# Performance work log

Measured on AMD Instinct MI355X. Metric: run time of the kernel, lower is better.

## Reference

```python
import jax, jax.numpy as jnp
import numpy as np

N_NODES, SEQ, FEAT, HID, NLAYERS = 126, 24, 17, 100, 2


def setup_inputs() -> dict:
    key = jax.random.key(0)
    ks = jax.random.split(key, 14)
    B = 64
    s = 1.0 / np.sqrt(HID)  # torch LSTM default init scale
    inp = {
        "x": jax.random.normal(ks[0], (B, SEQ, N_NODES, FEAT), dtype=jnp.float32),
        # per-node stacked LSTM weights, gate order (i, f, g, o) as in torch
        "W_ih0": jax.random.uniform(ks[1], (N_NODES, 4 * HID, FEAT), jnp.float32, -s, s),
        "W_hh0": jax.random.uniform(ks[2], (N_NODES, 4 * HID, HID), jnp.float32, -s, s),
        "b_ih0": jax.random.uniform(ks[3], (N_NODES, 4 * HID), jnp.float32, -s, s),
        "b_hh0": jax.random.uniform(ks[4], (N_NODES, 4 * HID), jnp.float32, -s, s),
        "W_ih1": jax.random.uniform(ks[5], (N_NODES, 4 * HID, HID), jnp.float32, -s, s),
        "W_hh1": jax.random.uniform(ks[6], (N_NODES, 4 * HID, HID), jnp.float32, -s, s),
        "b_ih1": jax.random.uniform(ks[7], (N_NODES, 4 * HID), jnp.float32, -s, s),
        "b_hh1": jax.random.uniform(ks[8], (N_NODES, 4 * HID), jnp.float32, -s, s),
        "w_lin": jax.random.uniform(ks[9], (1, HID), jnp.float32, -s, s),
        "b_lin": jax.random.uniform(ks[10], (1,), jnp.float32, -s, s),
        "w_end": jax.random.uniform(ks[11], (1, SEQ), jnp.float32, -0.2, 0.2),  # Conv2d(seqlen->1, k=1)
        "b_end": jax.random.uniform(ks[12], (1,), jnp.float32, -0.2, 0.2),
    }
    return inp


def _lstm_cell(xin, h, c, Wih, Whh, bih, bhh):
    # xin: [N,B,Fin], h/c: [N,B,H], Wih: [N,4H,Fin], Whh: [N,4H,H]
    g = (jnp.einsum("nbf,ngf->nbg", xin, Wih)
         + jnp.einsum("nbh,ngh->nbg", h, Whh)
         + (bih + bhh)[:, None, :])
    i, f, gg, o = jnp.split(g, 4, axis=-1)
    c_new = jax.nn.sigmoid(f) * c + jax.nn.sigmoid(i) * jnp.tanh(gg)
    h_new = jax.nn.sigmoid(o) * jnp.tanh(c_new)
    return h_new, c_new


def reference(x, W_ih0, W_hh0, b_ih0, b_hh0, W_ih1, W_hh1, b_ih1, b_hh1,
              w_lin, b_lin, w_end, b_end):
    B, T, N, F = x.shape
    H = W_hh0.shape[-1]
    xt = jnp.transpose(x, (1, 2, 0, 3))  # [T, N, B, F]
    z = jnp.zeros((N, B, H), dtype=x.dtype)

    def step(carry, x_t):
        h1, c1, h2, c2 = carry
        h1, c1 = _lstm_cell(x_t, h1, c1, W_ih0, W_hh0, b_ih0, b_hh0)
        h2, c2 = _lstm_cell(h1, h2, c2, W_ih1, W_hh1, b_ih1, b_hh1)
        return (h1, c1, h2, c2), h2

    (h1, c1, h2, c2), outs = jax.lax.scan(step, (z, z, z, z), xt)  # outs: [T,N,B,H]
    lin = jnp.einsum("tnbh,oh->tnbo", outs, w_lin) + b_lin  # [T,N,B,1]
    lstmlayer = jnp.transpose(lin, (2, 0, 1, 3))  # [B,T,N,1] (matches torch permute(2,1,0,3))
    # Conv2d(seqlen -> out_channels=1, kernel 1x1) over the T channel axis
    out = jnp.einsum("btnj,ct->bcnj", lstmlayer, w_end) + b_end[None, :, None, None]  # [B,1,N,1]
    hn = jnp.stack([h1, h2], axis=1)  # [N, num_layers=2, B, H]
    cn = jnp.stack([c1, c2], axis=1)
    return (out, hn, cn)
```

## Files before the change

kernel.cpp:

```cpp
#include <hip/hip_runtime.h>
#include <hip/hip_bf16.h>

#define NN 126
#define TT 24
#define FF 17
#define HH 100
#define NMT 25

#define AL_SH 51200
#define X0_SH AL_SH
#define X1_SH (AL_SH + 8192)
#define X0BUF 4096
#define X1BUF 7168
#define TOT_SH (X1_SH + 2 * X1BUF)
#define LDS_BYTES (TOT_SH * 2)

typedef __attribute__((ext_vector_type(8))) short short8v;
typedef __attribute__((ext_vector_type(4))) float float4v;

__device__ __forceinline__ short f2bf(float f) {
    union { float f; unsigned u; } v; v.f = f;
    unsigned r = v.u + 0x7FFFu + ((v.u >> 16) & 1u);
    return (short)(r >> 16);
}
#define LOG2E 1.4426950408889634f
__device__ __forceinline__ float sigm_(float x) {
    return __builtin_amdgcn_rcpf(1.0f + __builtin_amdgcn_exp2f(-LOG2E * x));
}
__device__ __forceinline__ float tanh_(float x) {
    return 1.0f - 2.0f * __builtin_amdgcn_rcpf(1.0f + __builtin_amdgcn_exp2f((2.0f * LOG2E) * x));
}

__global__ __launch_bounds__(1024, 4)
void lstm_skew(const float* __restrict__ x,
               const float* __restrict__ Wih0, const float* __restrict__ Whh0,
               const float* __restrict__ bih0, const float* __restrict__ bhh0,
               const float* __restrict__ Wih1, const float* __restrict__ Whh1,
               const float* __restrict__ bih1, const float* __restrict__ bhh1,
               const float* __restrict__ wlin, const float* __restrict__ blin,
               const float* __restrict__ wend, const float* __restrict__ bend,
               float* __restrict__ out)
{
    extern __shared__ short lds_s[];
    short* Al = lds_s;
    short* X0 = lds_s + X0_SH;
    short* X1 = lds_s + X1_SH;
    float* red = (float*)lds_s;

    const int n   = blockIdx.x >> 1;
    const int bh  = blockIdx.x & 1;
    const int tid = threadIdx.x, lane = tid & 63, w = tid >> 6;
    const int cl  = lane & 15, q = lane >> 4;
    const int mt0 = (w <= 8) ? (w * 2) : (18 + (w - 9));
    const int nmt = (w <= 8) ? 2 : 1;

    {
        const short8v zz = {0,0,0,0,0,0,0,0};
        for (int i = tid; i < TOT_SH / 8; i += 1024)
            *(short8v*)(lds_s + (size_t)i * 8) = zz;
    }
    __syncthreads();

    {
        const float* W = Whh0 + (size_t)n * 40000;
        for (int i = tid; i < 40000; i += 1024) {
            const int orl = i / 100, j = i - orl * 100;
            const int g = orl / 100, cell = orl - g * 100;
            const int gr = cell * 4 + g;
            const int k = 18 + j;
            Al[(((k >> 5) * NMT + (gr >> 4)) * 64 + ((((k >> 3) & 3) << 4) | (gr & 15))) * 8 + (k & 7)]
                = f2bf(W[i]);
        }
    }
    {
        const float* W = Wih0 + (size_t)n * 6800;
        for (int i = tid; i < 6800; i += 1024) {
            const int orl = i / 17, k = i - orl * 17;
            const int g = orl / 100, cell = orl - g * 100;
            const int gr = cell * 4 + g;
            Al[((gr >> 4) * 64 + ((((k >> 3) & 3) << 4) | (gr & 15))) * 8 + (k & 7)] = f2bf(W[i]);
        }
    }
    if (tid < 400) {
        const int g = tid / 100, cell = tid - g * 100;
        const int gr = cell * 4 + g;
        const int orow = n * 400 + tid;
        Al[((gr >> 4) * 64 + ((2 << 4) | (gr & 15))) * 8 + 1] = f2bf(bih0[orow] + bhh0[orow]);
    }

    short8v wreg[2][7];
    #pragma unroll
    for (int mi = 0; mi < 2; ++mi) {
        if (mi < nmt) {
            const int gr = (mt0 + mi) * 16 + cl;
            const int cell = gr >> 2, g = gr & 3;
            const int orow = n * 400 + g * HH + cell;
            const float* Wi = Wih1 + (size_t)orow * HH;
            const float* Wh = Whh1 + (size_t)orow * HH;
            #pragma unroll
            for (int kt = 0; kt < 7; ++kt) {
                const int k0 = kt * 32 + q * 8;
                float v[8];
                #pragma unroll
                for (int e = 0; e < 8; ++e) v[e] = 0.0f;
                if (k0 == 0) {
                    v[0] = bih1[orow] + bhh1[orow];
                    v[4] = Wi[0]; v[5] = Wi[1]; v[6] = Wi[2]; v[7] = Wi[3];
                } else if (k0 <= 96) {
                    #pragma unroll
                    for (int e = 0; e < 8; ++e) v[e] = Wi[k0 - 4 + e];
                } else if (k0 >= 104 && k0 <= 192) {
                    #pragma unroll
                    for (int e = 0; e < 8; ++e) v[e] = Wh[k0 - 104 + e];
                } else if (k0 == 200) {
                    v[0] = Wh[96]; v[1] = Wh[97]; v[2] = Wh[98]; v[3] = Wh[99];
                }
                short8v pv;
                #pragma unroll
                for (int e = 0; e < 8; ++e) pv[e] = f2bf(v[e]);
                wreg[mi][kt] = pv;
            }
        }
    }

    int aX0h1[2][2], aX1h1[2][2], aX1h2[2][2];
    #pragma unroll
    for (int mi = 0; mi < 2; ++mi) {
        const int cell = (mt0 + mi) * 4 + q;
        #pragma unroll
        for (int nh = 0; nh < 2; ++nh) {
            { const int k = 18 + cell;
              aX0h1[mi][nh] = (((k >> 5) * 2 + nh) * 64 + ((((k >> 3) & 3) << 4) | cl)) * 8 + (k & 7); }
            { const int k = 4 + cell;
              aX1h1[mi][nh] = (((k >> 5) * 2 + nh) * 64 + ((((k >> 3) & 3) << 4) | cl)) * 8 + (k & 7); }
            { const int k = 104 + cell;
              aX1h2[mi][nh] = (((k >> 5) * 2 + nh) * 64 + ((((k >> 3) & 3) << 4) | cl)) * 8 + (k & 7); }
        }
    }
    __syncthreads();

    if (tid < 32) {
        const int off = (((tid >> 4)) * 64 + (tid & 15)) * 8 + 0;
        X1[off] = (short)0x3F80;
        X1[X1BUF + off] = (short)0x3F80;
    }
    if (w < 2) {
        const int b = bh * 32 + w * 16 + cl;
        const float* xr = x + ((size_t)b * TT + 0) * (NN * FF) + n * FF;
        if (q < 2) {
            short8v pv;
            #pragma unroll
            for (int e = 0; e < 8; ++e) pv[e] = f2bf(xr[q * 8 + e]);
            *(short8v*)(X0 + ((size_t)w * 64 + lane) * 8) = pv;
        } else if (q == 2) {
            const unsigned lo = (unsigned short)f2bf(xr[16]);
            *(unsigned*)(X0 + ((size_t)w * 64 + lane) * 8) = (0x3F80u << 16) | lo;
        }
    }
    __syncthreads();

    float c1[2][2], c2[2][2], macc[2][2];
    #pragma unroll
    for (int mi = 0; mi < 2; ++mi)
        #pragma unroll
        for (int nh = 0; nh < 2; ++nh) { c1[mi][nh] = 0.f; c2[mi][nh] = 0.f; macc[mi][nh] = 0.f; }

    for (int i = 0; i <= TT; ++i) {
        const int rb = i & 1;
        const int wb = rb ^ 1;
        float4v acc[2][2];

        if (i < TT) {
            float xv0 = 0.f, xv1 = 0.f, xv2 = 0.f, xv3 = 0.f, xv4 = 0.f, xv5 = 0.f, xv6 = 0.f, xv7 = 0.f;
            const bool doX = (w < 2) && (i + 1 < TT);
            if (doX) {
                const int b = bh * 32 + w * 16 + cl;
                const float* xr = x + ((size_t)b * TT + (i + 1)) * (NN * FF) + n * FF;
                if (q < 2) {
                    const int k0 = q * 8;
                    xv0 = xr[k0 + 0]; xv1 = xr[k0 + 1]; xv2 = xr[k0 + 2]; xv3 = xr[k0 + 3];
                    xv4 = xr[k0 + 4]; xv5 = xr[k0 + 5]; xv6 = xr[k0 + 6]; xv7 = xr[k0 + 7];
                } else if (q == 2) {
                    xv0 = xr[16];
                }
            }

            #pragma unroll
            for (int mi = 0; mi < 2; ++mi) { acc[mi][0] = (float4v){0,0,0,0}; acc[mi][1] = (float4v){0,0,0,0}; }
            {
                const short* X0r = X0 + rb * X0BUF;
                #pragma unroll
                for (int kt = 0; kt < 4; ++kt) {
                    const short8v b0 = *(const short8v*)(X0r + (((size_t)kt * 2 + 0) * 64 + lane) * 8);
                    const short8v b1 = *(const short8v*)(X0r + (((size_t)kt * 2 + 1) * 64 + lane) * 8);
                    #pragma unroll
                    for (int mi = 0; mi < 2; ++mi) {
                        if (mi < nmt) {
                            const short8v a = *(const short8v*)(
                                Al + (((size_t)kt * NMT + (mt0 + mi)) * 64 + lane) * 8);
                            acc[mi][0] = __builtin_amdgcn_mfma_f32_16x16x32_bf16(a, b0, acc[mi][0], 0, 0, 0);
                            acc[mi][1] = __builtin_amdgcn_mfma_f32_16x16x32_bf16(a, b1, acc[mi][1], 0, 0, 0);
                        }
                    }
                }
            }
            const bool fin0 = (i == TT - 1);
            #pragma unroll
            for (int mi = 0; mi < 2; ++mi) {
                if (mi < nmt) {
                    const int cell = (mt0 + mi) * 4 + q;
                    #pragma unroll
                    for (int nh = 0; nh < 2; ++nh) {
                        const float iv = sigm_(acc[mi][nh][0]);
                        const float fv = sigm_(acc[mi][nh][1]);
                        const float gv = tanh_(acc[mi][nh][2]);
                        const float ov = sigm_(acc[mi][nh][3]);
                        const float c  = fv * c1[mi][nh] + iv * gv;
                        c1[mi][nh] = c;
                        const float h = ov * tanh_(c);
                        const short hb = f2bf(h);
                        X0[wb * X0BUF + aX0h1[mi][nh]] = hb;
                        X1[wb * X1BUF + aX1h1[mi][nh]] = hb;
                        if (fin0) {
                            const int b = bh * 32 + nh * 16 + cl;
                            out[8064 + ((size_t)(n * 2 + 0) * 64 + b) * HH + cell] = h;
                            out[8064 + 1612800 + ((size_t)(n * 2 + 0) * 64 + b) * HH + cell] = c;
                        }
                    }
                }
            }
            if (doX) {
                short* X0w = X0 + wb * X0BUF;
                if (q < 2) {
                    short8v pv;
                    pv[0] = f2bf(xv0); pv[1] = f2bf(xv1); pv[2] = f2bf(xv2); pv[3] = f2bf(xv3);
                    pv[4] = f2bf(xv4); pv[5] = f2bf(xv5); pv[6] = f2bf(xv6); pv[7] = f2bf(xv7);
                    *(short8v*)(X0w + ((size_t)w * 64 + lane) * 8) = pv;
                } else if (q == 2) {
                    const unsigned lo = (unsigned short)f2bf(xv0);
                    *(unsigned*)(X0w + ((size_t)w * 64 + lane) * 8) = (0x3F80u << 16) | lo;
                }
            }
        }

        if (i > 0) {
            #pragma unroll
            for (int mi = 0; mi < 2; ++mi) { acc[mi][0] = (float4v){0,0,0,0}; acc[mi][1] = (float4v){0,0,0,0}; }
            {
                const short* X1r = X1 + rb * X1BUF;
                #pragma unroll
                for (int kt = 0; kt < 7; ++kt) {
                    const short8v b0 = *(const short8v*)(X1r + (((size_t)kt * 2 + 0) * 64 + lane) * 8);
                    const short8v b1 = *(const short8v*)(X1r + (((size_t)kt * 2 + 1) * 64 + lane) * 8);
                    #pragma unroll
                    for (int mi = 0; mi < 2; ++mi) {
                        if (mi < nmt) {
                            acc[mi][0] = __builtin_amdgcn_mfma_f32_16x16x32_bf16(wreg[mi][kt], b0, acc[mi][0], 0, 0, 0);
                            acc[mi][1] = __builtin_amdgcn_mfma_f32_16x16x32_bf16(wreg[mi][kt], b1, acc[mi][1], 0, 0, 0);
                        }
                    }
                }
            }
            const float wet = wend[i - 1];
            const bool fin1 = (i == TT);
            #pragma unroll
            for (int mi = 0; mi < 2; ++mi) {
                if (mi < nmt) {
                    const int cell = (mt0 + mi) * 4 + q;
                    #pragma unroll
                    for (int nh = 0; nh < 2; ++nh) {
                        const float iv = sigm_(acc[mi][nh][0]);
                        const float fv = sigm_(acc[mi][nh][1]);
                        const float gv = tanh_(acc[mi][nh][2]);
                        const float ov = sigm_(acc[mi][nh][3]);
                        const float c  = fv * c2[mi][nh] + iv * gv;
                        c2[mi][nh] = c;
                        const float h = ov * tanh_(c);
                        macc[mi][nh] = fmaf(wet, h, macc[mi][nh]);
                        if (!fin1) X1[wb * X1BUF + aX1h2[mi][nh]] = f2bf(h);
                        if (fin1) {
                            const int b = bh * 32 + nh * 16 + cl;
                            out[8064 + ((size_t)(n * 2 + 1) * 64 + b) * HH + cell] = h;
                            out[8064 + 1612800 + ((size_t)(n * 2 + 1) * 64 + b) * HH + cell] = c;
                        }
                    }
                }
            }
        }
        __syncthreads();
    }

    #pragma unroll
    for (int mi = 0; mi < 2; ++mi) {
        if (mi < nmt) {
            const int cell = (mt0 + mi) * 4 + q;
            #pragma unroll
            for (int nh = 0; nh < 2; ++nh)
                red[cell * 32 + nh * 16 + cl] = wlin[cell] * macc[mi][nh];
        }
    }
    __syncthreads();
    if (tid < 32) {
        float s = 0.0f;
        for (int j = 0; j < HH; ++j) s += red[j * 32 + tid];
        float ws = 0.0f;
        for (int t2 = 0; t2 < TT; ++t2) ws += wend[t2];
        s += blin[0] * ws + bend[0];
        out[(size_t)(bh * 32 + tid) * NN + n] = s;
    }
}

extern "C" void kernel_launch(void* const* d_in, const int* in_sizes, int n_in,
                              void* d_out, int out_size, void* d_ws, size_t ws_size,
                              hipStream_t stream) {
    const float* x    = (const float*)d_in[0];
    const float* Wih0 = (const float*)d_in[1];
    const float* Whh0 = (const float*)d_in[2];
    const float* bih0 = (const float*)d_in[3];
    const float* bhh0 = (const float*)d_in[4];
    const float* Wih1 = (const float*)d_in[5];
    const float* Whh1 = (const float*)d_in[6];
    const float* bih1 = (const float*)d_in[7];
    const float* bhh1 = (const float*)d_in[8];
    const float* wlin = (const float*)d_in[9];
    const float* blin = (const float*)d_in[10];
    const float* wend = (const float*)d_in[11];
    const float* bend = (const float*)d_in[12];
    (void)d_ws; (void)ws_size; (void)in_sizes; (void)n_in; (void)out_size;

    lstm_skew<<<dim3(NN * 2), dim3(1024), LDS_BYTES, stream>>>(
        x, Wih0, Whh0, bih0, bhh0, Wih1, Whh1, bih1, bhh1,
        wlin, blin, wend, bend, (float*)d_out);
}
```

Before: 116.1 us.

## Halve block to 512 threads, give each wave more tiles, overlap layer MFMAs

Shrinks the block from 16 to 8 waves, so each wave owns 3 M-tiles (the last wave owns 4). Layer-1 weights for the extra tile are staged in a new LDS region instead of registers. Both layers' MFMA phases are now issued back-to-back before either gate activation, so the two matrix chains can interleave. This trades fewer waves and higher per-wave register pressure for more independent MFMA work per wave and less waiting between phases.

```diff
diff --git a/kernel.cpp b/kernel.cpp
--- a/kernel.cpp
+++ b/kernel.cpp
@@ -7,12 +7,13 @@
 #define HH 100
 #define NMT 25
 
-#define AL_SH 51200
-#define X0_SH AL_SH
-#define X1_SH (AL_SH + 8192)
+#define AL_SH   51200
+#define B24_SH  (AL_SH)
+#define X0_SH   (AL_SH + 3584)
+#define X1_SH   (X0_SH + 8192)
 #define X0BUF 4096
 #define X1BUF 7168
-#define TOT_SH (X1_SH + 2 * X1BUF)
+#define TOT_SH  (X1_SH + 2 * X1BUF)
 #define LDS_BYTES (TOT_SH * 2)
 
 typedef __attribute__((ext_vector_type(8))) short short8v;
@@ -31,39 +32,41 @@
     return 1.0f - 2.0f * __builtin_amdgcn_rcpf(1.0f + __builtin_amdgcn_exp2f((2.0f * LOG2E) * x));
 }
 
-__global__ __launch_bounds__(1024, 4)
-void lstm_skew(const float* __restrict__ x,
-               const float* __restrict__ Wih0, const float* __restrict__ Whh0,
-               const float* __restrict__ bih0, const float* __restrict__ bhh0,
-               const float* __restrict__ Wih1, const float* __restrict__ Whh1,
-               const float* __restrict__ bih1, const float* __restrict__ bhh1,
-               const float* __restrict__ wlin, const float* __restrict__ blin,
-               const float* __restrict__ wend, const float* __restrict__ bend,
-               float* __restrict__ out)
+__global__ __launch_bounds__(512, 2)
+void lstm_ovl(const float* __restrict__ x,
+              const float* __restrict__ Wih0, const float* __restrict__ Whh0,
+              const float* __restrict__ bih0, const float* __restrict__ bhh0,
+              const float* __restrict__ Wih1, const float* __restrict__ Whh1,
+              const float* __restrict__ bih1, const float* __restrict__ bhh1,
+              const float* __restrict__ wlin, const float* __restrict__ blin,
+              const float* __restrict__ wend, const float* __restrict__ bend,
+              float* __restrict__ out)
 {
     extern __shared__ short lds_s[];
-    short* Al = lds_s;
-    short* X0 = lds_s + X0_SH;
-    short* X1 = lds_s + X1_SH;
-    float* red = (float*)lds_s;
+    short* Al   = lds_s;
+    short* B24l = lds_s + B24_SH;
+    short* X0   = lds_s + X0_SH;
+    short* X1   = lds_s + X1_SH;
+    float* red  = (float*)lds_s;
 
     const int n   = blockIdx.x >> 1;
     const int bh  = blockIdx.x & 1;
     const int tid = threadIdx.x, lane = tid & 63, w = tid >> 6;
     const int cl  = lane & 15, q = lane >> 4;
-    const int mt0 = (w <= 8) ? (w * 2) : (18 + (w - 9));
-    const int nmt = (w <= 8) ? 2 : 1;
+    const int mt0 = w * 3;
+    const bool w7 = (w == 7);
+    const int nmt = w7 ? 4 : 3;
 
     {
         const short8v zz = {0,0,0,0,0,0,0,0};
-        for (int i = tid; i < TOT_SH / 8; i += 1024)
+        for (int i = tid; i < TOT_SH / 8; i += 512)
             *(short8v*)(lds_s + (size_t)i * 8) = zz;
     }
     __syncthreads();
 
     {
         const float* W = Whh0 + (size_t)n * 40000;
-        for (int i = tid; i < 40000; i += 1024) {
+        for (int i = tid; i < 40000; i += 512) {
             const int orl = i / 100, j = i - orl * 100;
             const int g = orl / 100, cell = orl - g * 100;
             const int gr = cell * 4 + g;
@@ -74,7 +77,7 @@
     }
     {
         const float* W = Wih0 + (size_t)n * 6800;
-        for (int i = tid; i < 6800; i += 1024) {
+        for (int i = tid; i < 6800; i += 512) {
             const int orl = i / 17, k = i - orl * 17;
             const int g = orl / 100, cell = orl - g * 100;
             const int gr = cell * 4 + g;
@@ -87,45 +90,63 @@
         const int orow = n * 400 + tid;
         Al[((gr >> 4) * 64 + ((2 << 4) | (gr & 15))) * 8 + 1] = f2bf(bih0[orow] + bhh0[orow]);
     }
-
-    short8v wreg[2][7];
+    for (int i = tid; i < 7 * 64; i += 512) {
+        const int kt = i >> 6, l = i & 63;
+        const int row16 = l & 15, kq = l >> 4;
+        const int gr = 24 * 16 + row16;
+        const int cell = gr >> 2, g = gr & 3;
+        const int orow = n * 400 + g * HH + cell;
+        const float* Wi = Wih1 + (size_t)orow * HH;
+        const float* Wh = Whh1 + (size_t)orow * HH;
+        short8v pv;
+        #pragma unroll
+        for (int e = 0; e < 8; ++e) {
+            const int k = kt * 32 + kq * 8 + e;
+            float f = 0.0f;
+            if (k == 0)                      f = bih1[orow] + bhh1[orow];
+            else if (k >= 4 && k < 4 + HH)   f = Wi[k - 4];
+            else if (k >= 104 && k < 104+HH) f = Wh[k - 104];
+            pv[e] = f2bf(f);
+        }
+        *(short8v*)(B24l + (size_t)i * 8) = pv;
+    }
+
+    short8v wr1[3][7];
     #pragma unroll
-    for (int mi = 0; mi < 2; ++mi) {
-        if (mi < nmt) {
-            const int gr = (mt0 + mi) * 16 + cl;
-            const int cell = gr >> 2, g = gr & 3;
-            const int orow = n * 400 + g * HH + cell;
-            const float* Wi = Wih1 + (size_t)orow * HH;
-            const float* Wh = Whh1 + (size_t)orow * HH;
-            #pragma unroll
-            for (int kt = 0; kt < 7; ++kt) {
-                const int k0 = kt * 32 + q * 8;
-                float v[8];
+    for (int mi = 0; mi < 3; ++mi) {
+        const int gr = (mt0 + mi) * 16 + cl;
+        const int cell = gr >> 2, g = gr & 3;
+        const int orow = n * 400 + g * HH + cell;
+        const float* Wi = Wih1 + (size_t)orow * HH;
+        const float* Wh = Whh1 + (size_t)orow * HH;
+        #pragma unroll
+        for (int kt = 0; kt < 7; ++kt) {
+            const int k0 = kt * 32 + q * 8;
+            float v[8];
+            #pragma unroll
+            for (int e = 0; e < 8; ++e) v[e] = 0.0f;
+            if (k0 == 0) {
+                v[0] = bih1[orow] + bhh1[orow];
+                v[4] = Wi[0]; v[5] = Wi[1]; v[6] = Wi[2]; v[7] = Wi[3];
+            } else if (k0 <= 96) {
                 #pragma unroll
-                for (int e = 0; e < 8; ++e) v[e] = 0.0f;
-                if (k0 == 0) {
-                    v[0] = bih1[orow] + bhh1[orow];
-                    v[4] = Wi[0]; v[5] = Wi[1]; v[6] = Wi[2]; v[7] = Wi[3];
-                } else if (k0 <= 96) {
-                    #pragma unroll
-                    for (int e = 0; e < 8; ++e) v[e] = Wi[k0 - 4 + e];
-                } else if (k0 >= 104 && k0 <= 192) {
-                    #pragma unroll
-                    for (int e = 0; e < 8; ++e) v[e] = Wh[k0 - 104 + e];
-                } else if (k0 == 200) {
-                    v[0] = Wh[96]; v[1] = Wh[97]; v[2] = Wh[98]; v[3] = Wh[99];
-                }
-                short8v pv;
+                for (int e = 0; e < 8; ++e) v[e] = Wi[k0 - 4 + e];
+            } else if (k0 >= 104 && k0 <= 192) {
                 #pragma unroll
-                for (int e = 0; e < 8; ++e) pv[e] = f2bf(v[e]);
-                wreg[mi][kt] = pv;
-            }
-        }
-    }
-
-    int aX0h1[2][2], aX1h1[2][2], aX1h2[2][2];
+                for (int e = 0; e < 8; ++e) v[e] = Wh[k0 - 104 + e];
+            } else if (k0 == 200) {
+                v[0] = Wh[96]; v[1] = Wh[97]; v[2] = Wh[98]; v[3] = Wh[99];
+            }
+            short8v pv;
+            #pragma unroll
+            for (int e = 0; e < 8; ++e) pv[e] = f2bf(v[e]);
+            wr1[mi][kt] = pv;
+        }
+    }
+
+    int aX0h1[4][2], aX1h1[4][2], aX1h2[4][2];
     #pragma unroll
-    for (int mi = 0; mi < 2; ++mi) {
+    for (int mi = 0; mi < 4; ++mi) {
         const int cell = (mt0 + mi) * 4 + q;
         #pragma unroll
         for (int nh = 0; nh < 2; ++nh) {
@@ -159,62 +180,87 @@
     }
     __syncthreads();
 
-    float c1[2][2], c2[2][2], macc[2][2];
+    float c1[4][2], c2[4][2], macc[4][2];
     #pragma unroll
-    for (int mi = 0; mi < 2; ++mi)
+    for (int mi = 0; mi < 4; ++mi)
         #pragma unroll
         for (int nh = 0; nh < 2; ++nh) { c1[mi][nh] = 0.f; c2[mi][nh] = 0.f; macc[mi][nh] = 0.f; }
 
     for (int i = 0; i <= TT; ++i) {
         const int rb = i & 1;
         const int wb = rb ^ 1;
-        float4v acc[2][2];
-
-        if (i < TT) {
-            float xv0 = 0.f, xv1 = 0.f, xv2 = 0.f, xv3 = 0.f, xv4 = 0.f, xv5 = 0.f, xv6 = 0.f, xv7 = 0.f;
-            const bool doX = (w < 2) && (i + 1 < TT);
-            if (doX) {
-                const int b = bh * 32 + w * 16 + cl;
-                const float* xr = x + ((size_t)b * TT + (i + 1)) * (NN * FF) + n * FF;
-                if (q < 2) {
-                    const int k0 = q * 8;
-                    xv0 = xr[k0 + 0]; xv1 = xr[k0 + 1]; xv2 = xr[k0 + 2]; xv3 = xr[k0 + 3];
-                    xv4 = xr[k0 + 4]; xv5 = xr[k0 + 5]; xv6 = xr[k0 + 6]; xv7 = xr[k0 + 7];
-                } else if (q == 2) {
-                    xv0 = xr[16];
-                }
-            }
-
-            #pragma unroll
-            for (int mi = 0; mi < 2; ++mi) { acc[mi][0] = (float4v){0,0,0,0}; acc[mi][1] = (float4v){0,0,0,0}; }
-            {
-                const short* X0r = X0 + rb * X0BUF;
+        float4v acc0[4][2], acc1[4][2];
+
+        const bool doL0 = (i < TT);
+        const bool doL1 = (i > 0);
+
+        float xv0 = 0.f, xv1 = 0.f, xv2 = 0.f, xv3 = 0.f, xv4 = 0.f, xv5 = 0.f, xv6 = 0.f, xv7 = 0.f;
+        const bool doX = doL0 && (w < 2) && (i + 1 < TT);
+        if (doX) {
+            const int b = bh * 32 + w * 16 + cl;
+            const float* xr = x + ((size_t)b * TT + (i + 1)) * (NN * FF) + n * FF;
+            if (q < 2) {
+                const int k0 = q * 8;
+                xv0 = xr[k0 + 0]; xv1 = xr[k0 + 1]; xv2 = xr[k0 + 2]; xv3 = xr[k0 + 3];
+                xv4 = xr[k0 + 4]; xv5 = xr[k0 + 5]; xv6 = xr[k0 + 6]; xv7 = xr[k0 + 7];
+            } else if (q == 2) {
+                xv0 = xr[16];
+            }
+        }
+
+        if (doL0) {
+            #pragma unroll
+            for (int mi = 0; mi < 4; ++mi) { acc0[mi][0] = (float4v){0,0,0,0}; acc0[mi][1] = (float4v){0,0,0,0}; }
+            const short* X0r = X0 + rb * X0BUF;
+            #pragma unroll
+            for (int kt = 0; kt < 4; ++kt) {
+                const short8v b0 = *(const short8v*)(X0r + (((size_t)kt * 2 + 0) * 64 + lane) * 8);
+                const short8v b1 = *(const short8v*)(X0r + (((size_t)kt * 2 + 1) * 64 + lane) * 8);
                 #pragma unroll
-                for (int kt = 0; kt < 4; ++kt) {
-                    const short8v b0 = *(const short8v*)(X0r + (((size_t)kt * 2 + 0) * 64 + lane) * 8);
-                    const short8v b1 = *(const short8v*)(X0r + (((size_t)kt * 2 + 1) * 64 + lane) * 8);
-                    #pragma unroll
-                    for (int mi = 0; mi < 2; ++mi) {
-                        if (mi < nmt) {
-                            const short8v a = *(const short8v*)(
-                                Al + (((size_t)kt * NMT + (mt0 + mi)) * 64 + lane) * 8);
-                            acc[mi][0] = __builtin_amdgcn_mfma_f32_16x16x32_bf16(a, b0, acc[mi][0], 0, 0, 0);
-                            acc[mi][1] = __builtin_amdgcn_mfma_f32_16x16x32_bf16(a, b1, acc[mi][1], 0, 0, 0);
-                        }
+                for (int mi = 0; mi < 4; ++mi) {
+                    if (mi < 3 || w7) {
+                        const short8v a = *(const short8v*)(
+                            Al + (((size_t)kt * NMT + (mt0 + mi)) * 64 + lane) * 8);
+                        acc0[mi][0] = __builtin_amdgcn_mfma_f32_16x16x32_bf16(a, b0, acc0[mi][0], 0, 0, 0);
+                        acc0[mi][1] = __builtin_amdgcn_mfma_f32_16x16x32_bf16(a, b1, acc0[mi][1], 0, 0, 0);
                     }
                 }
             }
+        }
+
+        if (doL1) {
+            #pragma unroll
+            for (int mi = 0; mi < 4; ++mi) { acc1[mi][0] = (float4v){0,0,0,0}; acc1[mi][1] = (float4v){0,0,0,0}; }
+            const short* X1r = X1 + rb * X1BUF;
+            #pragma unroll
+            for (int kt = 0; kt < 7; ++kt) {
+                const short8v b0 = *(const short8v*)(X1r + (((size_t)kt * 2 + 0) * 64 + lane) * 8);
+                const short8v b1 = *(const short8v*)(X1r + (((size_t)kt * 2 + 1) * 64 + lane) * 8);
+                #pragma unroll
+                for (int mi = 0; mi < 3; ++mi) {
+                    acc1[mi][0] = __builtin_amdgcn_mfma_f32_16x16x32_bf16(wr1[mi][kt], b0, acc1[mi][0], 0, 0, 0);
+                    acc1[mi][1] = __builtin_amdgcn_mfma_f32_16x16x32_bf16(wr1[mi][kt], b1, acc1[mi][1], 0, 0, 0);
+                }
+                if (w7) {
+                    const short8v a = *(const short8v*)(B24l + ((size_t)kt * 64 + lane) * 8);
+                    acc1[3][0] = __builtin_amdgcn_mfma_f32_16x16x32_bf16(a, b0, acc1[3][0], 0, 0, 0);
+                    acc1[3][1] = __builtin_amdgcn_mfma_f32_16x16x32_bf16(a, b1, acc1[3][1], 0, 0, 0);
+                }
+            }
+        }
+
+        if (doL0) {
             const bool fin0 = (i == TT - 1);
             #pragma unroll
-            for (int mi = 0; mi < 2; ++mi) {
-                if (mi < nmt) {
+            for (int mi = 0; mi < 4; ++mi) {
+                if (mi < 3 || w7) {
                     const int cell = (mt0 + mi) * 4 + q;
                     #pragma unroll
                     for (int nh = 0; nh < 2; ++nh) {
-                        const float iv = sigm_(acc[mi][nh][0]);
-                        const float fv = sigm_(acc[mi][nh][1]);
-                        const float gv = tanh_(acc[mi][nh][2]);
-                        const float ov = sigm_(acc[mi][nh][3]);
+                        const float iv = sigm_(acc0[mi][nh][0]);
+                        const float fv = sigm_(acc0[mi][nh][1]);
+                        const float gv = tanh_(acc0[mi][nh][2]);
+                        const float ov = sigm_(acc0[mi][nh][3]);
                         const float c  = fv * c1[mi][nh] + iv * gv;
                         c1[mi][nh] = c;
                         const float h = ov * tanh_(c);
@@ -243,36 +289,19 @@
             }
         }
 
-        if (i > 0) {
-            #pragma unroll
-            for (int mi = 0; mi < 2; ++mi) { acc[mi][0] = (float4v){0,0,0,0}; acc[mi][1] = (float4v){0,0,0,0}; }
-            {
-                const short* X1r = X1 + rb * X1BUF;
-                #pragma unroll
-                for (int kt = 0; kt < 7; ++kt) {
-                    const short8v b0 = *(const short8v*)(X1r + (((size_t)kt * 2 + 0) * 64 + lane) * 8);
-                    const short8v b1 = *(const short8v*)(X1r + (((size_t)kt * 2 + 1) * 64 + lane) * 8);
-                    #pragma unroll
-                    for (int mi = 0; mi < 2; ++mi) {
-                        if (mi < nmt) {
-                            acc[mi][0] = __builtin_amdgcn_mfma_f32_16x16x32_bf16(wreg[mi][kt], b0, acc[mi][0], 0, 0, 0);
-                            acc[mi][1] = __builtin_amdgcn_mfma_f32_16x16x32_bf16(wreg[mi][kt], b1, acc[mi][1], 0, 0, 0);
-                        }
-                    }
-                }
-            }
+        if (doL1) {
             const float wet = wend[i - 1];
             const bool fin1 = (i == TT);
             #pragma unroll
-            for (int mi = 0; mi < 2; ++mi) {
-                if (mi < nmt) {
+            for (int mi = 0; mi < 4; ++mi) {
+                if (mi < 3 || w7) {
                     const int cell = (mt0 + mi) * 4 + q;
                     #pragma unroll
                     for (int nh = 0; nh < 2; ++nh) {
-                        const float iv = sigm_(acc[mi][nh][0]);
-                        const float fv = sigm_(acc[mi][nh][1]);
-                        const float gv = tanh_(acc[mi][nh][2]);
-                        const float ov = sigm_(acc[mi][nh][3]);
+                        const float iv = sigm_(acc1[mi][nh][0]);
+                        const float fv = sigm_(acc1[mi][nh][1]);
+                        const float gv = tanh_(acc1[mi][nh][2]);
+                        const float ov = sigm_(acc1[mi][nh][3]);
                         const float c  = fv * c2[mi][nh] + iv * gv;
                         c2[mi][nh] = c;
                         const float h = ov * tanh_(c);
@@ -291,8 +320,8 @@
     }
 
     #pragma unroll
-    for (int mi = 0; mi < 2; ++mi) {
-        if (mi < nmt) {
+    for (int mi = 0; mi < 4; ++mi) {
+        if (mi < 3 || w7) {
             const int cell = (mt0 + mi) * 4 + q;
             #pragma unroll
             for (int nh = 0; nh < 2; ++nh)
@@ -328,7 +357,7 @@
     const float* bend = (const float*)d_in[12];
     (void)d_ws; (void)ws_size; (void)in_sizes; (void)n_in; (void)out_size;
 
-    lstm_skew<<<dim3(NN * 2), dim3(1024), LDS_BYTES, stream>>>(
+    lstm_ovl<<<dim3(NN * 2), dim3(512), LDS_BYTES, stream>>>(
         x, Wih0, Whh0, bih0, bhh0, Wih1, Whh1, bih1, bhh1,
         wlin, blin, wend, bend, (float*)d_out);
 }
```

Result: slower. 159.5 us (+37.3%).
